# Kernel optimization log

Measured on AMD Instinct MI355X. Metric: run time of the kernel, lower is better.

The kernel has to match this reference:

```python
import jax, jax.numpy as jnp
import numpy as np

KCONV = 4
NSTATE = 64
NH_SPA = 4
NH_SPE = 8
NH_ATTN = 8
QLEN = 5


def _ln(x, w, b, eps=1e-5):
    mu = jnp.mean(x, -1, keepdims=True)
    var = jnp.var(x, -1, keepdims=True)
    return (x - mu) * jax.lax.rsqrt(var + eps) * w + b


def _sincos_2d(dim, H):
    # standard 2D sin-cos positional embedding, [H*H, dim]
    def e1(d, pos):
        omega = 1.0 / (10000.0 ** (np.arange(d // 2, dtype=np.float64) / (d / 2.0)))
        out = pos[:, None] * omega[None, :]
        return np.concatenate([np.sin(out), np.cos(out)], axis=-1)
    gh, gw = np.meshgrid(np.arange(H), np.arange(H), indexing='ij')
    emb = np.concatenate([e1(dim // 2, gh.reshape(-1)), e1(dim // 2, gw.reshape(-1))], axis=-1)
    return jnp.asarray(emb, jnp.float32)


def _ssd_scan(x, dt, A, Bm, Cm):
    # x:[b,l,h,p] dt:[b,l,h] A:[h] Bm,Cm:[b,l,n] (ngroups=1)
    b, l, h, p = x.shape
    dA = jnp.exp(dt * A)            # [b,l,h]
    dtx = dt[..., None] * x          # [b,l,h,p]

    def step(hs, inp):
        dA_t, dtx_t, B_t, C_t = inp
        hs = hs * dA_t[:, :, None, None] + dtx_t[..., None] * B_t[:, None, None, :]
        return hs, jnp.einsum('bhpn,bn->bhp', hs, C_t)

    h0 = jnp.zeros((b, h, p, Bm.shape[-1]), x.dtype)
    _, ys = jax.lax.scan(step, h0, (dA.transpose(1, 0, 2), dtx.transpose(1, 0, 2, 3),
                                    Bm.transpose(1, 0, 2), Cm.transpose(1, 0, 2)))
    return ys.transpose(1, 0, 2, 3)


def _mamba2(u, in_w, conv_w, conv_b, dt_bias, A_log, Dp, rms_w, out_w, nheads, n=NSTATE):
    # Mamba2 forward (d_state=64, d_conv=4, expand=2, rmsnorm gated, no biases on projections)
    b, l, _ = u.shape
    d_in_proj = in_w.shape[0]
    d_inner = (d_in_proj - 2 * n - nheads) // 2
    zxbcdt = u @ in_w.T
    z = zxbcdt[..., :d_inner]
    xBC = zxbcdt[..., d_inner:2 * d_inner + 2 * n]
    dt = jax.nn.softplus(zxbcdt[..., 2 * d_inner + 2 * n:] + dt_bias)  # [b,l,h]
    # causal depthwise conv1d, kernel 4
    xp = jnp.pad(xBC, ((0, 0), (KCONV - 1, 0), (0, 0)))
    xc = sum(xp[:, k:k + l, :] * conv_w[:, k] for k in range(KCONV)) + conv_b
    xBC = jax.nn.silu(xc)
    xh = xBC[..., :d_inner].reshape(b, l, nheads, -1)
    Bm = xBC[..., d_inner:d_inner + n]
    Cm = xBC[..., d_inner + n:]
    y = _ssd_scan(xh, dt, -jnp.exp(A_log), Bm, Cm)
    y = y + Dp[None, None, :, None] * xh
    y = y.reshape(b, l, -1) * jax.nn.silu(z)
    y = y * jax.lax.rsqrt(jnp.mean(y * y, -1, keepdims=True) + 1e-5) * rms_w
    return y @ out_w.T


def _forward(floats, sorted_index):
    (x, spa_ln_w, spa_ln_b, spa_in_w, spa_conv_w, spa_conv_b, spa_dt_bias, spa_A_log, spa_D,
     spa_rms_w, spa_out_w, spe_ln_w, spe_ln_b, spe_in_w, spe_conv_w, spe_conv_b, spe_dt_bias,
     spe_A_log, spe_D, spe_rms_w, spe_out_w, norm_w, norm_b, cprj_w, cprj_b,
     aq_w, aq_b, ak_w, ak_b, av_w, av_b, ao_w, ao_b,
     sq_w, sq_b, sk_w, sk_b, sv_w, sv_b, so_w, so_b,
     ds_conv_w, ds_ln_w, ds_ln_b) = floats
    b, c, H, W = x.shape
    # seq_generate: pos embed + reorder by (precomputed MST/BFS) sorted_index
    pe = _sincos_2d(c, H)                                  # [H*W, c]
    xs = x.transpose(0, 2, 3, 1).reshape(b, H * W, c) + pe[None]
    xs = jnp.take_along_axis(xs, sorted_index[..., None], axis=1)
    # SSD blocks
    for i in range(spa_ln_w.shape[0]):
        h1 = _mamba2(_ln(xs, spa_ln_w[i], spa_ln_b[i]), spa_in_w[i], spa_conv_w[i], spa_conv_b[i],
                     spa_dt_bias[i], spa_A_log[i], spa_D[i], spa_rms_w[i], spa_out_w[i], NH_SPA) + xs
        h2 = _mamba2(_ln(h1.transpose(0, 2, 1), spe_ln_w[i], spe_ln_b[i]), spe_in_w[i], spe_conv_w[i],
                     spe_conv_b[i], spe_dt_bias[i], spe_A_log[i], spe_D[i], spe_rms_w[i], spe_out_w[i], NH_SPE)
        xs = h2.transpose(0, 2, 1) + h1
    xs = _ln(xs, norm_w, norm_b)
    # center query: Conv1d(kernel=QLEN, pad=0) over the first QLEN tokens -> [b, c]
    center = jnp.einsum('blc,ocl->bo', xs[:, :QLEN, :], cprj_w) + cprj_b
    # Spa_Attention: center query attends over all tokens; per-token reweighting of V
    nh = NH_ATTN
    hd = c // nh
    q = (center @ aq_w.T + aq_b).reshape(b, nh, hd)
    k = (xs @ ak_w.T + ak_b).reshape(b, -1, nh, hd)
    v = (xs @ av_w.T + av_b).reshape(b, -1, nh, hd)
    attn = jax.nn.softmax(jnp.einsum('bhd,blhd->bhl', q, k) / float(np.sqrt(hd)), axis=-1)
    out = (v * attn.transpose(0, 2, 1)[..., None]).reshape(b, -1, c) @ ao_w.T + ao_b
    xs = xs + out
    # Spe_Attention: self-attention over channel tokens (dim = seq_len)
    xt = xs.transpose(0, 2, 1)                              # [b, c, L]
    q2 = xt @ sq_w.T + sq_b
    k2 = xt @ sk_w.T + sk_b
    v2 = xt @ sv_w.T + sv_b
    attn2 = jax.nn.softmax(jnp.einsum('bqd,bkd->bqk', q2, k2) / float(np.sqrt(xt.shape[-1])), axis=-1)
    xs = xs + ((attn2 @ v2) @ so_w.T + so_b).transpose(0, 2, 1)
    # Downsample: invert ordering, reshape to image, conv stride 2, LayerNorm
    inv = jnp.argsort(sorted_index, axis=1)
    xr = jnp.take_along_axis(xs, inv[..., None], axis=1).reshape(b, H, W, c)
    y = jax.lax.conv_general_dilated(xr, ds_conv_w, (2, 2), [(1, 1), (1, 1)],
                                     dimension_numbers=('NHWC', 'HWIO', 'NHWC'))
    return _ln(y, ds_ln_w, ds_ln_b)  # [b, H/2, W/2, c]


def setup_inputs() -> dict:
    key = jax.random.key(0)
    ks = iter(jax.random.split(key, 64))

    def rn(shape, s=0.02):
        return jax.random.normal(next(ks), shape, jnp.float32) * s

    d = {}
    d['x'] = jax.random.normal(next(ks), (16, 128, 16, 16), jnp.float32)
    d['sorted_index'] = jnp.argsort(jax.random.uniform(next(ks), (16, 256)), axis=1)
    d['spa_ln_w'] = jnp.ones((2, 128), jnp.float32)
    d['spa_ln_b'] = jnp.zeros((2, 128), jnp.float32)
    d['spa_in_w'] = rn((2, 644, 128))
    d['spa_conv_w'] = rn((2, 384, 4), 0.2)
    d['spa_conv_b'] = jnp.zeros((2, 384), jnp.float32)
    d['spa_dt_bias'] = rn((2, 4), 0.1) - 2.0
    d['spa_A_log'] = jnp.log(jax.random.uniform(next(ks), (2, 4), minval=1.0, maxval=8.0))
    d['spa_D'] = jnp.ones((2, 4), jnp.float32)
    d['spa_rms_w'] = jnp.ones((2, 256), jnp.float32)
    d['spa_out_w'] = rn((2, 128, 256))
    d['spe_ln_w'] = jnp.ones((2, 256), jnp.float32)
    d['spe_ln_b'] = jnp.zeros((2, 256), jnp.float32)
    d['spe_in_w'] = rn((2, 1160, 256))
    d['spe_conv_w'] = rn((2, 640, 4), 0.2)
    d['spe_conv_b'] = jnp.zeros((2, 640), jnp.float32)
    d['spe_dt_bias'] = rn((2, 8), 0.1) - 2.0
    d['spe_A_log'] = jnp.log(jax.random.uniform(next(ks), (2, 8), minval=1.0, maxval=8.0))
    d['spe_D'] = jnp.ones((2, 8), jnp.float32)
    d['spe_rms_w'] = jnp.ones((2, 512), jnp.float32)
    d['spe_out_w'] = rn((2, 256, 512))
    d['norm_w'] = jnp.ones((128,), jnp.float32)
    d['norm_b'] = jnp.zeros((128,), jnp.float32)
    d['cprj_w'] = rn((128, 128, 5), 0.05)
    d['cprj_b'] = jnp.zeros((128,), jnp.float32)
    for nm in ['aq', 'ak', 'av', 'ao']:
        d[nm + '_w'] = rn((128, 128), 0.05)
        d[nm + '_b'] = jnp.zeros((128,), jnp.float32)
    for nm in ['sq', 'sk', 'sv', 'so']:
        d[nm + '_w'] = rn((256, 256), 0.05)
        d[nm + '_b'] = jnp.zeros((256,), jnp.float32)
    d['ds_conv_w'] = rn((3, 3, 128, 128), 0.05)
    d['ds_ln_w'] = jnp.ones((128,), jnp.float32)
    d['ds_ln_b'] = jnp.zeros((128,), jnp.float32)
    return d


def reference(x, sorted_index, spa_ln_w, spa_ln_b, spa_in_w, spa_conv_w, spa_conv_b, spa_dt_bias,
              spa_A_log, spa_D, spa_rms_w, spa_out_w, spe_ln_w, spe_ln_b, spe_in_w, spe_conv_w,
              spe_conv_b, spe_dt_bias, spe_A_log, spe_D, spe_rms_w, spe_out_w, norm_w, norm_b,
              cprj_w, cprj_b, aq_w, aq_b, ak_w, ak_b, av_w, av_b, ao_w, ao_b,
              sq_w, sq_b, sk_w, sk_b, sv_w, sv_b, so_w, so_b, ds_conv_w, ds_ln_w, ds_ln_b):
    floats = (x, spa_ln_w, spa_ln_b, spa_in_w, spa_conv_w, spa_conv_b, spa_dt_bias, spa_A_log, spa_D,
              spa_rms_w, spa_out_w, spe_ln_w, spe_ln_b, spe_in_w, spe_conv_w, spe_conv_b, spe_dt_bias,
              spe_A_log, spe_D, spe_rms_w, spe_out_w, norm_w, norm_b, cprj_w, cprj_b,
              aq_w, aq_b, ak_w, ak_b, av_w, av_b, ao_w, ao_b,
              sq_w, sq_b, sk_w, sk_b, sv_w, sv_b, so_w, so_b, ds_conv_w, ds_ln_w, ds_ln_b)
    return _forward(floats, sorted_index)
```

## Files before the change

kernel.cpp:

```cpp
#include <hip/hip_runtime.h>
#include <math.h>

#define DEV __device__ __forceinline__

DEV float siluf(float x){ return x / (1.f + __expf(-x)); }
DEV float softplusf(float x){ return (x > 20.f) ? x : log1pf(__expf(x)); }

DEV void blk_sum2(float &a, float &b, float* sm){
    int lane = threadIdx.x & 63, wid = threadIdx.x >> 6, nw = blockDim.x >> 6;
    #pragma unroll
    for (int off = 32; off; off >>= 1){ a += __shfl_down(a, off); b += __shfl_down(b, off); }
    if (lane == 0){ sm[wid] = a; sm[8 + wid] = b; }
    __syncthreads();
    float ra = 0.f, rb = 0.f;
    for (int i = 0; i < nw; i++){ ra += sm[i]; rb += sm[8 + i]; }
    __syncthreads();
    a = ra; b = rb;
}
DEV float blk_sum1(float v, float* sm){
    int lane = threadIdx.x & 63, wid = threadIdx.x >> 6, nw = blockDim.x >> 6;
    #pragma unroll
    for (int off = 32; off; off >>= 1) v += __shfl_down(v, off);
    if (lane == 0) sm[wid] = v;
    __syncthreads();
    float r = 0.f;
    for (int i = 0; i < nw; i++) r += sm[i];
    __syncthreads();
    return r;
}
DEV float blk_max1(float v, float* sm){
    int lane = threadIdx.x & 63, wid = threadIdx.x >> 6, nw = blockDim.x >> 6;
    #pragma unroll
    for (int off = 32; off; off >>= 1) v = fmaxf(v, __shfl_down(v, off));
    if (lane == 0) sm[wid] = v;
    __syncthreads();
    float r = -3.4e38f;
    for (int i = 0; i < nw; i++) r = fmaxf(r, sm[i]);
    __syncthreads();
    return r;
}

DEV void tr_body(const float* __restrict__ ip, float* __restrict__ op,
                 int R, int C, int c0, int r0){
    __shared__ float tile[32][33];
    int tx = threadIdx.x & 31, ty = threadIdx.x >> 5;
    #pragma unroll
    for (int rr = ty; rr < 32; rr += 8)
        tile[rr][tx] = ip[(size_t)(r0 + rr) * C + c0 + tx];
    __syncthreads();
    #pragma unroll
    for (int rr = ty; rr < 32; rr += 8)
        op[(size_t)(c0 + rr) * R + r0 + tx] = tile[tx][rr];
}

__global__ __launch_bounds__(256) void k_tr(const float* __restrict__ in,
                                            float* __restrict__ out, int R, int C){
    tr_body(in + (size_t)blockIdx.z * R * C, out + (size_t)blockIdx.z * R * C,
            R, C, blockIdx.x * 32, blockIdx.y * 32);
}

__global__ __launch_bounds__(256) void k_tr_multi(const float* __restrict__ x,
        float* __restrict__ xT, const float* __restrict__ aow, float* __restrict__ owt,
        const float* __restrict__ sow, float* __restrict__ sowt){
    int idx = blockIdx.x;
    if (idx < 512){
        int bx = idx & 7, by = (idx >> 3) & 3, bz = idx >> 5;
        tr_body(x + (size_t)bz * 32768, xT + (size_t)bz * 32768, 128, 256, bx * 32, by * 32);
    } else if (idx < 528){
        int l = idx - 512;
        tr_body(aow, owt, 128, 128, (l & 3) * 32, (l >> 2) * 32);
    } else {
        int l = idx - 528;
        tr_body(sow, sowt, 256, 256, (l & 7) * 32, (l >> 3) * 32);
    }
}

__global__ void k_embed(const float* __restrict__ xT, const int* __restrict__ sidx,
                        float* __restrict__ xs){
    int bl = blockIdx.x; int b = bl >> 8; int c = threadIdx.x;
    int p = sidx[bl];
    int hh = p >> 4, ww = p & 15;
    int pos = (c < 64) ? hh : ww;
    int jm = c & 63;
    float om = __expf(-(float)(jm & 31) * 0.28782313662425574f);
    float ang = (float)pos * om;
    float pe = (jm < 32) ? sinf(ang) : cosf(ang);
    xs[(size_t)bl * 128 + c] = xT[((size_t)(b * 256 + p)) * 128 + c] + pe;
}

__global__ void k_ln(const float* __restrict__ in, const float* __restrict__ w,
                     const float* __restrict__ bb, float* __restrict__ out, int dim){
    __shared__ float sm[16];
    int row = blockIdx.x, t = threadIdx.x;
    float v = in[(size_t)row * dim + t];
    float a = v, q = v * v;
    blk_sum2(a, q, sm);
    float inv = 1.f / (float)dim;
    float mu = a * inv;
    float var = q * inv - mu * mu;
    float rs = rsqrtf(var + 1e-5f);
    out[(size_t)row * dim + t] = (v - mu) * rs * w[t] + bb[t];
}

__global__ __launch_bounds__(256) void k_gemm_ln(const float* __restrict__ A,
        const float* __restrict__ W, const float* __restrict__ lw,
        const float* __restrict__ lb, float* __restrict__ out, int N, int K){
    __shared__ float lds[2][32][68];
    int j0 = blockIdx.x * 64, r0 = blockIdx.y * 64;
    int tid = threadIdx.x;
    int cg = tid & 15, rg = tid >> 4;
    int row = tid >> 2, kg = tid & 3;
    int wrow = j0 + row; if (wrow > N - 1) wrow = N - 1;
    const float* Ar = A + (size_t)(r0 + row) * K;
    float s = 0.f, ss = 0.f;
    for (int k0 = 0; k0 < K; k0 += 32){
        float4 a0 = *(const float4*)(Ar + k0 + kg * 4);
        float4 a1 = *(const float4*)(Ar + k0 + 16 + kg * 4);
        s  += a0.x + a0.y + a0.z + a0.w + a1.x + a1.y + a1.z + a1.w;
        ss += a0.x*a0.x + a0.y*a0.y + a0.z*a0.z + a0.w*a0.w
            + a1.x*a1.x + a1.y*a1.y + a1.z*a1.z + a1.w*a1.w;
    }
    s  += __shfl_xor(s, 1);  ss += __shfl_xor(ss, 1);
    s  += __shfl_xor(s, 2);  ss += __shfl_xor(ss, 2);
    float inv = 1.f / (float)K;
    float mu = s * inv;
    float rs = rsqrtf(ss * inv - mu * mu + 1e-5f);
    float acc[4][4] = {};
    for (int k0 = 0; k0 < K; k0 += 32){
        float4 a0 = *(const float4*)(Ar + k0 + kg * 4);
        float4 a1 = *(const float4*)(Ar + k0 + 16 + kg * 4);
        float4 w0 = *(const float4*)(lw + k0 + kg * 4);
        float4 w1 = *(const float4*)(lw + k0 + 16 + kg * 4);
        float4 b0 = *(const float4*)(lb + k0 + kg * 4);
        float4 b1 = *(const float4*)(lb + k0 + 16 + kg * 4);
        const float* Wp = W + (size_t)wrow * K + k0 + kg * 4;
        float4 v0 = *(const float4*)(Wp);
        float4 v1 = *(const float4*)(Wp + 16);
        a0.x = (a0.x - mu) * rs * w0.x + b0.x; a0.y = (a0.y - mu) * rs * w0.y + b0.y;
        a0.z = (a0.z - mu) * rs * w0.z + b0.z; a0.w = (a0.w - mu) * rs * w0.w + b0.w;
        a1.x = (a1.x - mu) * rs * w1.x + b1.x; a1.y = (a1.y - mu) * rs * w1.y + b1.y;
        a1.z = (a1.z - mu) * rs * w1.z + b1.z; a1.w = (a1.w - mu) * rs * w1.w + b1.w;
        __syncthreads();
        lds[0][kg * 4 + 0][row] = a0.x; lds[0][kg * 4 + 1][row] = a0.y;
        lds[0][kg * 4 + 2][row] = a0.z; lds[0][kg * 4 + 3][row] = a0.w;
        lds[0][16 + kg * 4 + 0][row] = a1.x; lds[0][16 + kg * 4 + 1][row] = a1.y;
        lds[0][16 + kg * 4 + 2][row] = a1.z; lds[0][16 + kg * 4 + 3][row] = a1.w;
        lds[1][kg * 4 + 0][row] = v0.x; lds[1][kg * 4 + 1][row] = v0.y;
        lds[1][kg * 4 + 2][row] = v0.z; lds[1][kg * 4 + 3][row] = v0.w;
        lds[1][16 + kg * 4 + 0][row] = v1.x; lds[1][16 + kg * 4 + 1][row] = v1.y;
        lds[1][16 + kg * 4 + 2][row] = v1.z; lds[1][16 + kg * 4 + 3][row] = v1.w;
        __syncthreads();
        #pragma unroll
        for (int kk = 0; kk < 32; kk++){
            float4 a4 = *(const float4*)(&lds[0][kk][rg << 2]);
            float4 w4 = *(const float4*)(&lds[1][kk][cg << 2]);
            float av_[4] = {a4.x, a4.y, a4.z, a4.w};
            float wv_[4] = {w4.x, w4.y, w4.z, w4.w};
            #pragma unroll
            for (int ri = 0; ri < 4; ri++)
                #pragma unroll
                for (int ci = 0; ci < 4; ci++)
                    acc[ri][ci] = fmaf(av_[ri], wv_[ci], acc[ri][ci]);
        }
    }
    #pragma unroll
    for (int ri = 0; ri < 4; ri++){
        int r = r0 + (rg << 2) + ri;
        int j = j0 + (cg << 2);
        if (j < N){
            float4 v = make_float4(acc[ri][0], acc[ri][1], acc[ri][2], acc[ri][3]);
            *(float4*)(&out[(size_t)r * N + j]) = v;
        }
    }
}

__global__ __launch_bounds__(256) void k_gemm_gate(const float* __restrict__ Y,
        const float* __restrict__ Z, const float* __restrict__ rw,
        const float* __restrict__ W, const float* __restrict__ res,
        float* __restrict__ out, int N, int K, int zs, int mode){
    __shared__ float lds[2][32][68];
    __shared__ float sscale[64];
    int j0 = blockIdx.x * 64, r0 = blockIdx.y * 64;
    int tid = threadIdx.x;
    int cg = tid & 15, rg = tid >> 4;
    int row = tid >> 2, kg = tid & 3;
    const float* Yr = Y + (size_t)(r0 + row) * K;
    const float* Zr = Z + (size_t)(r0 + row) * zs;
    float ssq = 0.f;
    float acc[4][4] = {};
    for (int k0 = 0; k0 < K; k0 += 32){
        float4 y0 = *(const float4*)(Yr + k0 + kg * 4);
        float4 y1 = *(const float4*)(Yr + k0 + 16 + kg * 4);
        float4 z0 = *(const float4*)(Zr + k0 + kg * 4);
        float4 z1 = *(const float4*)(Zr + k0 + 16 + kg * 4);
        float4 g0 = *(const float4*)(rw + k0 + kg * 4);
        float4 g1 = *(const float4*)(rw + k0 + 16 + kg * 4);
        const float* Wp = W + (size_t)(j0 + row) * K + k0 + kg * 4;
        float4 v0 = *(const float4*)(Wp);
        float4 v1 = *(const float4*)(Wp + 16);
        y0.x *= siluf(z0.x); y0.y *= siluf(z0.y); y0.z *= siluf(z0.z); y0.w *= siluf(z0.w);
        y1.x *= siluf(z1.x); y1.y *= siluf(z1.y); y1.z *= siluf(z1.z); y1.w *= siluf(z1.w);
        ssq += y0.x*y0.x + y0.y*y0.y + y0.z*y0.z + y0.w*y0.w
             + y1.x*y1.x + y1.y*y1.y + y1.z*y1.z + y1.w*y1.w;
        y0.x *= g0.x; y0.y *= g0.y; y0.z *= g0.z; y0.w *= g0.w;
        y1.x *= g1.x; y1.y *= g1.y; y1.z *= g1.z; y1.w *= g1.w;
        __syncthreads();
        lds[0][kg * 4 + 0][row] = y0.x; lds[0][kg * 4 + 1][row] = y0.y;
        lds[0][kg * 4 + 2][row] = y0.z; lds[0][kg * 4 + 3][row] = y0.w;
        lds[0][16 + kg * 4 + 0][row] = y1.x; lds[0][16 + kg * 4 + 1][row] = y1.y;
        lds[0][16 + kg * 4 + 2][row] = y1.z; lds[0][16 + kg * 4 + 3][row] = y1.w;
        lds[1][kg * 4 + 0][row] = v0.x; lds[1][kg * 4 + 1][row] = v0.y;
        lds[1][kg * 4 + 2][row] = v0.z; lds[1][kg * 4 + 3][row] = v0.w;
        lds[1][16 + kg * 4 + 0][row] = v1.x; lds[1][16 + kg * 4 + 1][row] = v1.y;
        lds[1][16 + kg * 4 + 2][row] = v1.z; lds[1][16 + kg * 4 + 3][row] = v1.w;
        __syncthreads();
        #pragma unroll
        for (int kk = 0; kk < 32; kk++){
            float4 a4 = *(const float4*)(&lds[0][kk][rg << 2]);
            float4 w4 = *(const float4*)(&lds[1][kk][cg << 2]);
            float av_[4] = {a4.x, a4.y, a4.z, a4.w};
            float wv_[4] = {w4.x, w4.y, w4.z, w4.w};
            #pragma unroll
            for (int ri = 0; ri < 4; ri++)
                #pragma unroll
                for (int ci = 0; ci < 4; ci++)
                    acc[ri][ci] = fmaf(av_[ri], wv_[ci], acc[ri][ci]);
        }
    }
    ssq += __shfl_xor(ssq, 1);
    ssq += __shfl_xor(ssq, 2);
    if ((tid & 3) == 0) sscale[row] = rsqrtf(ssq / (float)K + 1e-5f);
    __syncthreads();
    if (mode == 2){
        float (*T)[68] = (float (*)[68])lds;
        #pragma unroll
        for (int ri = 0; ri < 4; ri++){
            float sc = sscale[(rg << 2) + ri];
            #pragma unroll
            for (int ci = 0; ci < 4; ci++)
                T[(cg << 2) + ci][(rg << 2) + ri] = acc[ri][ci] * sc;
        }
        __syncthreads();
        int b2 = r0 >> 7, ii0 = r0 & 127;
        int jj = tid >> 2, seg = tid & 3;
        size_t base = ((size_t)(b2 * 256 + j0 + jj)) * 128 + ii0 + seg * 16;
        float* op = out + base;
        const float* rp = res + base;
        #pragma unroll
        for (int c = 0; c < 4; c++){
            float4 v = *(const float4*)(&T[jj][seg * 16 + c * 4]);
            float4 rv = *(const float4*)(rp + c * 4);
            v.x += rv.x; v.y += rv.y; v.z += rv.z; v.w += rv.w;
            *(float4*)(op + c * 4) = v;
        }
    } else {
        #pragma unroll
        for (int ri = 0; ri < 4; ri++){
            int r = r0 + (rg << 2) + ri;
            int j = j0 + (cg << 2);
            float sc = sscale[(rg << 2) + ri];
            float4 v = make_float4(acc[ri][0] * sc, acc[ri][1] * sc,
                                   acc[ri][2] * sc, acc[ri][3] * sc);
            float4 rv = *(const float4*)(&res[(size_t)r * N + j]);
            v.x += rv.x; v.y += rv.y; v.z += rv.z; v.w += rv.w;
            *(float4*)(&out[(size_t)r * N + j]) = v;
        }
    }
}

DEV void gemm_core(const float* __restrict__ A, const float* __restrict__ W,
                   const float* __restrict__ bias, float* __restrict__ out,
                   int N, int K, int mode, int j0, int r0){
    __shared__ float lds[2][32][68];
    int tid = threadIdx.x;
    int cg = tid & 15, rg = tid >> 4;
    int row = tid >> 2, kg = tid & 3;
    int wrow = j0 + row; if (wrow > N - 1) wrow = N - 1;
    float acc[4][4] = {};
    for (int k0 = 0; k0 < K; k0 += 32){
        const float* Ap = A + (size_t)(r0 + row) * K + k0 + kg * 4;
        float4 a0 = *(const float4*)(Ap);
        float4 a1 = *(const float4*)(Ap + 16);
        const float* Wp = W + (size_t)wrow * K + k0 + kg * 4;
        float4 w0 = *(const float4*)(Wp);
        float4 w1 = *(const float4*)(Wp + 16);
        __syncthreads();
        lds[0][kg * 4 + 0][row] = a0.x; lds[0][kg * 4 + 1][row] = a0.y;
        lds[0][kg * 4 + 2][row] = a0.z; lds[0][kg * 4 + 3][row] = a0.w;
        lds[0][16 + kg * 4 + 0][row] = a1.x; lds[0][16 + kg * 4 + 1][row] = a1.y;
        lds[0][16 + kg * 4 + 2][row] = a1.z; lds[0][16 + kg * 4 + 3][row] = a1.w;
        lds[1][kg * 4 + 0][row] = w0.x; lds[1][kg * 4 + 1][row] = w0.y;
        lds[1][kg * 4 + 2][row] = w0.z; lds[1][kg * 4 + 3][row] = w0.w;
        lds[1][16 + kg * 4 + 0][row] = w1.x; lds[1][16 + kg * 4 + 1][row] = w1.y;
        lds[1][16 + kg * 4 + 2][row] = w1.z; lds[1][16 + kg * 4 + 3][row] = w1.w;
        __syncthreads();
        #pragma unroll
        for (int kk = 0; kk < 32; kk++){
            float4 a4 = *(const float4*)(&lds[0][kk][rg << 2]);
            float4 w4 = *(const float4*)(&lds[1][kk][cg << 2]);
            float av_[4] = {a4.x, a4.y, a4.z, a4.w};
            float wv_[4] = {w4.x, w4.y, w4.z, w4.w};
            #pragma unroll
            for (int ri = 0; ri < 4; ri++)
                #pragma unroll
                for (int ci = 0; ci < 4; ci++)
                    acc[ri][ci] = fmaf(av_[ri], wv_[ci], acc[ri][ci]);
        }
    }
    if (mode == 3){
        float (*T)[68] = (float (*)[68])lds;
        __syncthreads();
        #pragma unroll
        for (int ri = 0; ri < 4; ri++)
            #pragma unroll
            for (int ci = 0; ci < 4; ci++)
                T[(cg << 2) + ci][(rg << 2) + ri] = acc[ri][ci];
        __syncthreads();
        int b2 = r0 >> 7, ii0 = r0 & 127;
        int jj = tid >> 2, seg = tid & 3;
        size_t base = ((size_t)(b2 * 256 + j0 + jj)) * 128 + ii0 + seg * 16;
        float* op = out + base;
        float bj = bias[j0 + jj];
        #pragma unroll
        for (int c = 0; c < 4; c++){
            float4 v = *(const float4*)(&T[jj][seg * 16 + c * 4]);
            v.x += bj; v.y += bj; v.z += bj; v.w += bj;
            *(float4*)(op + c * 4) = v;
        }
    } else {
        #pragma unroll
        for (int ri = 0; ri < 4; ri++){
            int r = r0 + (rg << 2) + ri;
            int j = j0 + (cg << 2);
            float4 v = make_float4(acc[ri][0], acc[ri][1], acc[ri][2], acc[ri][3]);
            v.x += bias[j]; v.y += bias[j + 1]; v.z += bias[j + 2]; v.w += bias[j + 3];
            *(float4*)(&out[(size_t)r * N + j]) = v;
        }
    }
}

struct GJob { const float* W; const float* bias; float* out; int mode; };

__global__ __launch_bounds__(256) void k_gemm3(const float* __restrict__ A,
                                               GJob ja, GJob jb, GJob jc,
                                               int N, int K){
    GJob j = (blockIdx.z == 0) ? ja : ((blockIdx.z == 1) ? jb : jc);
    gemm_core(A, j.W, j.bias, j.out, N, K, j.mode, blockIdx.x * 64, blockIdx.y * 64);
}

__global__ void k_conv(const float* __restrict__ zx, const float* __restrict__ cw,
                       const float* __restrict__ cb, float* __restrict__ xc,
                       const float* __restrict__ dtbias, const float* __restrict__ Al,
                       float* __restrict__ dt, float* __restrict__ dlA,
                       int L, int D, int stride, int off, int nh, int dtoff){
    int bl = blockIdx.x;
    int l = bl & (L - 1);
    const float* base = zx + (size_t)bl * stride + off;
    for (int d = threadIdx.x; d < D; d += blockDim.x){
        float acc = cb[d];
        #pragma unroll
        for (int k = 0; k < 4; k++){
            int dl = l + k - 3;
            if (dl >= 0) acc += base[(ptrdiff_t)(k - 3) * stride + d] * cw[d * 4 + k];
        }
        xc[(size_t)bl * D + d] = siluf(acc);
    }
    int t = threadIdx.x;
    if (t < nh){
        float xv = zx[(size_t)bl * stride + dtoff + t] + dtbias[t];
        float d = softplusf(xv);
        dt[(size_t)bl * nh + t] = d;
        dlA[(size_t)bl * nh + t] = -d * __expf(Al[t]);
    }
}

__global__ __launch_bounds__(256) void k_ssd_chunk(
        const float* __restrict__ xc, const float* __restrict__ dt,
        const float* __restrict__ dlA, float* __restrict__ y,
        float* __restrict__ S, float* __restrict__ clb,
        int L, int nh, int nc, int xcs, int bo, int co, int ys){
    __shared__ float sX[64][68];
    __shared__ float sB[64][68];
    __shared__ float sC[64][68];
    __shared__ float cl[64], sdt[64], sw[64];
    int blk = blockIdx.x;
    int c = blk % nc; int bh = blk / nc; int h = bh % nh; int b = bh / nh;
    int l0 = c * 64;
    int tid = threadIdx.x;
    const float* base = xc + ((size_t)(b * L + l0)) * xcs;
    for (int idx = tid; idx < 4096; idx += 256){
        int s = idx >> 6, n = idx & 63;
        const float* row = base + (size_t)s * xcs;
        sX[s][n] = row[h * 64 + n];
        sB[s][n] = row[bo + n];
        sC[s][n] = row[co + n];
    }
    if (tid < 64){
        size_t di = (size_t)(b * L + l0 + tid) * nh + h;
        float dlv = dlA[di];
        sdt[tid] = dt[di];
// ... 260 lines not shown
        for (int ii = 0; ii < 8; ii++)
            sa[ii][t] = (lgp[0][ii][t] + lgp[1][ii][t]) * (1.f / 16.f);
    }
    __syncthreads();
    if (t < 8){
        float mx = -3.4e38f;
        for (int j = 0; j < 128; j++) mx = fmaxf(mx, sa[t][j]);
        float sm = 0.f;
        for (int j = 0; j < 128; j++) sm += __expf(sa[t][j] - mx);
        mxs[t] = mx; sms[t] = 1.f / sm;
    }
    __syncthreads();
    if (t < 128){
        #pragma unroll
        for (int ii = 0; ii < 8; ii++)
            sa[ii][t] = __expf(sa[ii][t] - mxs[ii]) * sms[ii];
    }
    __syncthreads();
    {
        float acc[8] = {};
        const float* vb = v2 + (size_t)b * 32768 + t;
        for (int j = 0; j < 128; j++){
            float vv = vb[(size_t)j * 256];
            #pragma unroll
            for (int ii = 0; ii < 8; ii++) acc[ii] = fmaf(sa[ii][j], vv, acc[ii]);
        }
        #pragma unroll
        for (int ii = 0; ii < 8; ii++) av[ii][t] = acc[ii];
    }
    __syncthreads();
    float acc[8] = {};
    for (int d = 0; d < 256; d++){
        float wv = sowt[d * 256 + t];
        #pragma unroll
        for (int ii = 0; ii < 8; ii++) acc[ii] = fmaf(av[ii][d], wv, acc[ii]);
    }
    float bias = sob[t];
    int p = sidx[b * 256 + t];
    const float* xin = xs + ((size_t)(b * 256 + t)) * 128 + i0;
    float* xout = xr + ((size_t)(b * 256 + p)) * 128 + i0;
    #pragma unroll
    for (int ii = 0; ii < 8; ii++) xout[ii] = xin[ii] + acc[ii] + bias;
}

__global__ __launch_bounds__(256) void k_conv_gemm(const float* __restrict__ xr,
                                                   const float* __restrict__ W2,
                                                   float* __restrict__ part){
    __shared__ float As[16][68];
    __shared__ float Ws[16][64];
    int j0 = blockIdx.x * 64, r0 = blockIdx.y * 64, s = blockIdx.z;
    int tid = threadIdx.x;
    int cg = tid & 15, rg = tid >> 4;
    int arow = tid >> 2, akg = tid & 3;
    int r = r0 + arow; int b = r >> 6, oh = (r >> 3) & 7, ow = r & 7;
    float acc[4][4] = {};
    int kbeg = s * 288, kend = kbeg + 288;
    for (int k0 = kbeg; k0 < kend; k0 += 16){
        {
            int k = k0 + akg * 4;
            int khw = k >> 7, c = k & 127;
            int kh = khw / 3, kw = khw - kh * 3;
            int ih = oh * 2 - 1 + kh, iw = ow * 2 - 1 + kw;
            float4 a4 = make_float4(0.f, 0.f, 0.f, 0.f);
            if (ih >= 0 && ih < 16 && iw >= 0 && iw < 16)
                a4 = *(const float4*)(xr + ((size_t)((b << 8) + (ih << 4) + iw)) * 128 + c);
            As[akg * 4 + 0][arow] = a4.x; As[akg * 4 + 1][arow] = a4.y;
            As[akg * 4 + 2][arow] = a4.z; As[akg * 4 + 3][arow] = a4.w;
        }
        #pragma unroll
        for (int it = 0; it < 4; it++){
            int idx = tid + it * 256;
            int jj = idx & 63, kk = idx >> 6;
            Ws[kk][jj] = W2[(size_t)(k0 + kk) * 128 + j0 + jj];
        }
        __syncthreads();
        #pragma unroll
        for (int kk = 0; kk < 16; kk++){
            float4 a4 = *(const float4*)(&As[kk][rg << 2]);
            float4 w4 = *(const float4*)(&Ws[kk][cg << 2]);
            float av_[4] = {a4.x, a4.y, a4.z, a4.w};
            float wv_[4] = {w4.x, w4.y, w4.z, w4.w};
            #pragma unroll
            for (int ri = 0; ri < 4; ri++)
                #pragma unroll
                for (int ci = 0; ci < 4; ci++)
                    acc[ri][ci] = fmaf(av_[ri], wv_[ci], acc[ri][ci]);
        }
        __syncthreads();
    }
    float* pp = part + (size_t)s * 1024 * 128;
    #pragma unroll
    for (int ri = 0; ri < 4; ri++){
        int rr = r0 + (rg << 2) + ri;
        #pragma unroll
        for (int ci = 0; ci < 4; ci++){
            int j = j0 + (cg << 2) + ci;
            pp[(size_t)rr * 128 + j] = acc[ri][ci];
        }
    }
}

__global__ void k_part_ln(const float* __restrict__ part, const float* __restrict__ lnw,
                          const float* __restrict__ lnb, float* __restrict__ out){
    __shared__ float sm[16];
    int r = blockIdx.x, t = threadIdx.x;
    float v = part[(size_t)r * 128 + t]
            + part[(size_t)(1024 + r) * 128 + t]
            + part[(size_t)(2048 + r) * 128 + t]
            + part[(size_t)(3072 + r) * 128 + t];
    float a = v, q = v * v;
    blk_sum2(a, q, sm);
    float mu = a * (1.f / 128.f);
    float var = q * (1.f / 128.f) - mu * mu;
    float rs = rsqrtf(var + 1e-5f);
    out[(size_t)r * 128 + t] = (v - mu) * rs * lnw[t] + lnb[t];
}

extern "C" void kernel_launch(void* const* d_in, const int* in_sizes, int n_in,
                              void* d_out, int out_size, void* d_ws, size_t ws_size,
                              hipStream_t stream) {
    const float* x          = (const float*)d_in[0];
    const int*   sidx       = (const int*)  d_in[1];
    const float* spa_ln_w   = (const float*)d_in[2];
    const float* spa_ln_b   = (const float*)d_in[3];
    const float* spa_in_w   = (const float*)d_in[4];
    const float* spa_conv_w = (const float*)d_in[5];
    const float* spa_conv_b = (const float*)d_in[6];
    const float* spa_dt_bias= (const float*)d_in[7];
    const float* spa_A_log  = (const float*)d_in[8];
    const float* spa_D      = (const float*)d_in[9];
    const float* spa_rms_w  = (const float*)d_in[10];
    const float* spa_out_w  = (const float*)d_in[11];
    const float* spe_ln_w   = (const float*)d_in[12];
    const float* spe_ln_b   = (const float*)d_in[13];
    const float* spe_in_w   = (const float*)d_in[14];
    const float* spe_conv_w = (const float*)d_in[15];
    const float* spe_conv_b = (const float*)d_in[16];
    const float* spe_dt_bias= (const float*)d_in[17];
    const float* spe_A_log  = (const float*)d_in[18];
    const float* spe_D      = (const float*)d_in[19];
    const float* spe_rms_w  = (const float*)d_in[20];
// ... 106 lines not shown
```

Baseline: 639.4 us.

## Use bf16 MFMA in projection GEMMs and prefetch conv GEMM tiles

Replaces the FP32 scalar-FMA inner loops of the LN-fused GEMM, the gated RMSNorm GEMM and the three-way QKV GEMM with bf16 MFMA 16x16x32 matrix instructions. Operands are converted to bf16 in shared memory, the K step is widened to 64, and the epilogues are remapped to the MFMA accumulator layout. Separately, the downsample conv GEMM now uses register prefetch of the next A/W tile and float4 weight loads. The bf16 conversion lowers GEMM input precision and may loosen numerical accuracy against the FP32 reference.

After: 549.0 us. -14.1%, faster.

```diff
diff --git a/kernel.cpp b/kernel.cpp
--- a/kernel.cpp
+++ b/kernel.cpp
@@ -3,8 +3,21 @@
 
 #define DEV __device__ __forceinline__
 
+typedef __attribute__((ext_vector_type(8))) short short8;
+typedef __attribute__((ext_vector_type(4))) float f32x4;
+typedef unsigned short ushort_t;
+typedef unsigned int uint_t;
+
 DEV float siluf(float x){ return x / (1.f + __expf(-x)); }
 DEV float softplusf(float x){ return (x > 20.f) ? x : log1pf(__expf(x)); }
+
+DEV ushort_t bf16r(float f){
+    uint_t u = __float_as_uint(f);
+    return (ushort_t)((u + 0x7fffu + ((u >> 16) & 1u)) >> 16);
+}
+DEV uint_t pack2(float a, float b){
+    return (uint_t)bf16r(a) | ((uint_t)bf16r(b) << 16);
+}
 
 DEV void blk_sum2(float &a, float &b, float* sm){
     int lane = threadIdx.x & 63, wid = threadIdx.x >> 6, nw = blockDim.x >> 6;
@@ -102,16 +115,19 @@
     out[(size_t)row * dim + t] = (v - mu) * rs * w[t] + bb[t];
 }
 
+
 __global__ __launch_bounds__(256) void k_gemm_ln(const float* __restrict__ A,
         const float* __restrict__ W, const float* __restrict__ lw,
         const float* __restrict__ lb, float* __restrict__ out, int N, int K){
-    __shared__ float lds[2][32][68];
+    __shared__ __align__(16) ushort_t smem[2 * 64 * 72];
+    ushort_t (*Abf)[72] = (ushort_t (*)[72])smem;
+    ushort_t (*Wbf)[72] = (ushort_t (*)[72])(smem + 64 * 72);
     int j0 = blockIdx.x * 64, r0 = blockIdx.y * 64;
     int tid = threadIdx.x;
-    int cg = tid & 15, rg = tid >> 4;
     int row = tid >> 2, kg = tid & 3;
     int wrow = j0 + row; if (wrow > N - 1) wrow = N - 1;
     const float* Ar = A + (size_t)(r0 + row) * K;
+    const float* Wr = W + (size_t)wrow * K;
     float s = 0.f, ss = 0.f;
     for (int k0 = 0; k0 < K; k0 += 32){
         float4 a0 = *(const float4*)(Ar + k0 + kg * 4);
@@ -125,51 +141,61 @@
     float inv = 1.f / (float)K;
     float mu = s * inv;
     float rs = rsqrtf(ss * inv - mu * mu + 1e-5f);
-    float acc[4][4] = {};
-    for (int k0 = 0; k0 < K; k0 += 32){
-        float4 a0 = *(const float4*)(Ar + k0 + kg * 4);
-        float4 a1 = *(const float4*)(Ar + k0 + 16 + kg * 4);
-        float4 w0 = *(const float4*)(lw + k0 + kg * 4);
-        float4 w1 = *(const float4*)(lw + k0 + 16 + kg * 4);
-        float4 b0 = *(const float4*)(lb + k0 + kg * 4);
-        float4 b1 = *(const float4*)(lb + k0 + 16 + kg * 4);
-        const float* Wp = W + (size_t)wrow * K + k0 + kg * 4;
-        float4 v0 = *(const float4*)(Wp);
-        float4 v1 = *(const float4*)(Wp + 16);
-        a0.x = (a0.x - mu) * rs * w0.x + b0.x; a0.y = (a0.y - mu) * rs * w0.y + b0.y;
-        a0.z = (a0.z - mu) * rs * w0.z + b0.z; a0.w = (a0.w - mu) * rs * w0.w + b0.w;
-        a1.x = (a1.x - mu) * rs * w1.x + b1.x; a1.y = (a1.y - mu) * rs * w1.y + b1.y;
-        a1.z = (a1.z - mu) * rs * w1.z + b1.z; a1.w = (a1.w - mu) * rs * w1.w + b1.w;
-        __syncthreads();
-        lds[0][kg * 4 + 0][row] = a0.x; lds[0][kg * 4 + 1][row] = a0.y;
-        lds[0][kg * 4 + 2][row] = a0.z; lds[0][kg * 4 + 3][row] = a0.w;
-        lds[0][16 + kg * 4 + 0][row] = a1.x; lds[0][16 + kg * 4 + 1][row] = a1.y;
-        lds[0][16 + kg * 4 + 2][row] = a1.z; lds[0][16 + kg * 4 + 3][row] = a1.w;
-        lds[1][kg * 4 + 0][row] = v0.x; lds[1][kg * 4 + 1][row] = v0.y;
-        lds[1][kg * 4 + 2][row] = v0.z; lds[1][kg * 4 + 3][row] = v0.w;
-        lds[1][16 + kg * 4 + 0][row] = v1.x; lds[1][16 + kg * 4 + 1][row] = v1.y;
-        lds[1][16 + kg * 4 + 2][row] = v1.z; lds[1][16 + kg * 4 + 3][row] = v1.w;
-        __syncthreads();
-        #pragma unroll
-        for (int kk = 0; kk < 32; kk++){
-            float4 a4 = *(const float4*)(&lds[0][kk][rg << 2]);
-            float4 w4 = *(const float4*)(&lds[1][kk][cg << 2]);
-            float av_[4] = {a4.x, a4.y, a4.z, a4.w};
-            float wv_[4] = {w4.x, w4.y, w4.z, w4.w};
-            #pragma unroll
-            for (int ri = 0; ri < 4; ri++)
-                #pragma unroll
-                for (int ci = 0; ci < 4; ci++)
-                    acc[ri][ci] = fmaf(av_[ri], wv_[ci], acc[ri][ci]);
-        }
-    }
-    #pragma unroll
-    for (int ri = 0; ri < 4; ri++){
-        int r = r0 + (rg << 2) + ri;
-        int j = j0 + (cg << 2);
+    int wv = tid >> 6, lane = tid & 63, lm = lane & 15, quad = lane >> 4;
+    f32x4 zero4 = {0.f, 0.f, 0.f, 0.f};
+    f32x4 acc[4] = {zero4, zero4, zero4, zero4};
+    for (int kc0 = 0; kc0 < K; kc0 += 64){
+        int kb = kc0 + kg * 16;
+        float4 q[4], g[4], b[4], p[4];
+        #pragma unroll
+        for (int i = 0; i < 4; i++){
+            q[i] = *(const float4*)(Ar + kb + i * 4);
+            g[i] = *(const float4*)(lw + kb + i * 4);
+            b[i] = *(const float4*)(lb + kb + i * 4);
+            p[i] = *(const float4*)(Wr + kb + i * 4);
+        }
+        #pragma unroll
+        for (int i = 0; i < 4; i++){
+            q[i].x = (q[i].x - mu) * rs * g[i].x + b[i].x;
+            q[i].y = (q[i].y - mu) * rs * g[i].y + b[i].y;
+            q[i].z = (q[i].z - mu) * rs * g[i].z + b[i].z;
+            q[i].w = (q[i].w - mu) * rs * g[i].w + b[i].w;
+        }
+        __syncthreads();
+        {
+            uint4 u0, u1;
+            u0.x = pack2(q[0].x, q[0].y); u0.y = pack2(q[0].z, q[0].w);
+            u0.z = pack2(q[1].x, q[1].y); u0.w = pack2(q[1].z, q[1].w);
+            u1.x = pack2(q[2].x, q[2].y); u1.y = pack2(q[2].z, q[2].w);
+            u1.z = pack2(q[3].x, q[3].y); u1.w = pack2(q[3].z, q[3].w);
+            *(uint4*)&Abf[row][kg * 16] = u0;
+            *(uint4*)&Abf[row][kg * 16 + 8] = u1;
+            u0.x = pack2(p[0].x, p[0].y); u0.y = pack2(p[0].z, p[0].w);
+            u0.z = pack2(p[1].x, p[1].y); u0.w = pack2(p[1].z, p[1].w);
+            u1.x = pack2(p[2].x, p[2].y); u1.y = pack2(p[2].z, p[2].w);
+            u1.z = pack2(p[3].x, p[3].y); u1.w = pack2(p[3].z, p[3].w);
+            *(uint4*)&Wbf[row][kg * 16] = u0;
+            *(uint4*)&Wbf[row][kg * 16 + 8] = u1;
+        }
+        __syncthreads();
+        #pragma unroll
+        for (int kk = 0; kk < 64; kk += 32){
+            short8 af = *(const short8*)&Abf[wv * 16 + lm][kk + quad * 8];
+            #pragma unroll
+            for (int c = 0; c < 4; c++){
+                short8 bfv = *(const short8*)&Wbf[c * 16 + lm][kk + quad * 8];
+                acc[c] = __builtin_amdgcn_mfma_f32_16x16x32_bf16(af, bfv, acc[c], 0, 0, 0);
+            }
+        }
+    }
+    int rbase = r0 + wv * 16 + quad * 4;
+    #pragma unroll
+    for (int c = 0; c < 4; c++){
+        int j = j0 + c * 16 + lm;
         if (j < N){
-            float4 v = make_float4(acc[ri][0], acc[ri][1], acc[ri][2], acc[ri][3]);
-            *(float4*)(&out[(size_t)r * N + j]) = v;
+            #pragma unroll
+            for (int reg = 0; reg < 4; reg++)
+                out[(size_t)(rbase + reg) * N + j] = acc[c][reg];
         }
     }
 }
@@ -178,68 +204,79 @@
         const float* __restrict__ Z, const float* __restrict__ rw,
         const float* __restrict__ W, const float* __restrict__ res,
         float* __restrict__ out, int N, int K, int zs, int mode){
-    __shared__ float lds[2][32][68];
+    __shared__ __align__(16) ushort_t smem[2 * 64 * 72];
+    ushort_t (*Abf)[72] = (ushort_t (*)[72])smem;
+    ushort_t (*Wbf)[72] = (ushort_t (*)[72])(smem + 64 * 72);
     __shared__ float sscale[64];
     int j0 = blockIdx.x * 64, r0 = blockIdx.y * 64;
     int tid = threadIdx.x;
-    int cg = tid & 15, rg = tid >> 4;
     int row = tid >> 2, kg = tid & 3;
     const float* Yr = Y + (size_t)(r0 + row) * K;
     const float* Zr = Z + (size_t)(r0 + row) * zs;
+    const float* Wr = W + (size_t)(j0 + row) * K;
+    int wv = tid >> 6, lane = tid & 63, lm = lane & 15, quad = lane >> 4;
     float ssq = 0.f;
-    float acc[4][4] = {};
-    for (int k0 = 0; k0 < K; k0 += 32){
-        float4 y0 = *(const float4*)(Yr + k0 + kg * 4);
-        float4 y1 = *(const float4*)(Yr + k0 + 16 + kg * 4);
-        float4 z0 = *(const float4*)(Zr + k0 + kg * 4);
-        float4 z1 = *(const float4*)(Zr + k0 + 16 + kg * 4);
-        float4 g0 = *(const float4*)(rw + k0 + kg * 4);
-        float4 g1 = *(const float4*)(rw + k0 + 16 + kg * 4);
-        const float* Wp = W + (size_t)(j0 + row) * K + k0 + kg * 4;
-        float4 v0 = *(const float4*)(Wp);
-        float4 v1 = *(const float4*)(Wp + 16);
-        y0.x *= siluf(z0.x); y0.y *= siluf(z0.y); y0.z *= siluf(z0.z); y0.w *= siluf(z0.w);
-        y1.x *= siluf(z1.x); y1.y *= siluf(z1.y); y1.z *= siluf(z1.z); y1.w *= siluf(z1.w);
-        ssq += y0.x*y0.x + y0.y*y0.y + y0.z*y0.z + y0.w*y0.w
-             + y1.x*y1.x + y1.y*y1.y + y1.z*y1.z + y1.w*y1.w;
-        y0.x *= g0.x; y0.y *= g0.y; y0.z *= g0.z; y0.w *= g0.w;
-        y1.x *= g1.x; y1.y *= g1.y; y1.z *= g1.z; y1.w *= g1.w;
-        __syncthreads();
-        lds[0][kg * 4 + 0][row] = y0.x; lds[0][kg * 4 + 1][row] = y0.y;
-        lds[0][kg * 4 + 2][row] = y0.z; lds[0][kg * 4 + 3][row] = y0.w;
-        lds[0][16 + kg * 4 + 0][row] = y1.x; lds[0][16 + kg * 4 + 1][row] = y1.y;
-        lds[0][16 + kg * 4 + 2][row] = y1.z; lds[0][16 + kg * 4 + 3][row] = y1.w;
-        lds[1][kg * 4 + 0][row] = v0.x; lds[1][kg * 4 + 1][row] = v0.y;
-        lds[1][kg * 4 + 2][row] = v0.z; lds[1][kg * 4 + 3][row] = v0.w;
-        lds[1][16 + kg * 4 + 0][row] = v1.x; lds[1][16 + kg * 4 + 1][row] = v1.y;
-        lds[1][16 + kg * 4 + 2][row] = v1.z; lds[1][16 + kg * 4 + 3][row] = v1.w;
-        __syncthreads();
-        #pragma unroll
-        for (int kk = 0; kk < 32; kk++){
-            float4 a4 = *(const float4*)(&lds[0][kk][rg << 2]);
-            float4 w4 = *(const float4*)(&lds[1][kk][cg << 2]);
-            float av_[4] = {a4.x, a4.y, a4.z, a4.w};
-            float wv_[4] = {w4.x, w4.y, w4.z, w4.w};
-            #pragma unroll
-            for (int ri = 0; ri < 4; ri++)
-                #pragma unroll
-                for (int ci = 0; ci < 4; ci++)
-                    acc[ri][ci] = fmaf(av_[ri], wv_[ci], acc[ri][ci]);
+    f32x4 zero4 = {0.f, 0.f, 0.f, 0.f};
+    f32x4 acc[4] = {zero4, zero4, zero4, zero4};
+    for (int kc0 = 0; kc0 < K; kc0 += 64){
+        int kb = kc0 + kg * 16;
+        float4 y[4], z[4], g[4], p[4];
+        #pragma unroll
+        for (int i = 0; i < 4; i++){
+            y[i] = *(const float4*)(Yr + kb + i * 4);
+            z[i] = *(const float4*)(Zr + kb + i * 4);
+            g[i] = *(const float4*)(rw + kb + i * 4);
+            p[i] = *(const float4*)(Wr + kb + i * 4);
+        }
+        #pragma unroll
+        for (int i = 0; i < 4; i++){
+            y[i].x *= siluf(z[i].x); y[i].y *= siluf(z[i].y);
+            y[i].z *= siluf(z[i].z); y[i].w *= siluf(z[i].w);
+            ssq += y[i].x*y[i].x + y[i].y*y[i].y + y[i].z*y[i].z + y[i].w*y[i].w;
+            y[i].x *= g[i].x; y[i].y *= g[i].y; y[i].z *= g[i].z; y[i].w *= g[i].w;
+        }
+        __syncthreads();
+        {
+            uint4 u0, u1;
+            u0.x = pack2(y[0].x, y[0].y); u0.y = pack2(y[0].z, y[0].w);
+            u0.z = pack2(y[1].x, y[1].y); u0.w = pack2(y[1].z, y[1].w);
+            u1.x = pack2(y[2].x, y[2].y); u1.y = pack2(y[2].z, y[2].w);
+            u1.z = pack2(y[3].x, y[3].y); u1.w = pack2(y[3].z, y[3].w);
+            *(uint4*)&Abf[row][kg * 16] = u0;
+            *(uint4*)&Abf[row][kg * 16 + 8] = u1;
+            u0.x = pack2(p[0].x, p[0].y); u0.y = pack2(p[0].z, p[0].w);
+            u0.z = pack2(p[1].x, p[1].y); u0.w = pack2(p[1].z, p[1].w);
+            u1.x = pack2(p[2].x, p[2].y); u1.y = pack2(p[2].z, p[2].w);
+            u1.z = pack2(p[3].x, p[3].y); u1.w = pack2(p[3].z, p[3].w);
+            *(uint4*)&Wbf[row][kg * 16] = u0;
+            *(uint4*)&Wbf[row][kg * 16 + 8] = u1;
+        }
+        __syncthreads();
+        #pragma unroll
+        for (int kk = 0; kk < 64; kk += 32){
+            short8 af = *(const short8*)&Abf[wv * 16 + lm][kk + quad * 8];
+            #pragma unroll
+            for (int c = 0; c < 4; c++){
+                short8 bfv = *(const short8*)&Wbf[c * 16 + lm][kk + quad * 8];
+                acc[c] = __builtin_amdgcn_mfma_f32_16x16x32_bf16(af, bfv, acc[c], 0, 0, 0);
+            }
         }
     }
     ssq += __shfl_xor(ssq, 1);
     ssq += __shfl_xor(ssq, 2);
-    if ((tid & 3) == 0) sscale[row] = rsqrtf(ssq / (float)K + 1e-5f);
-    __syncthreads();
+    if (kg == 0) sscale[row] = rsqrtf(ssq / (float)K + 1e-5f);
+    __syncthreads();
+    int lr0 = wv * 16 + quad * 4;
+    float scr[4];
+    #pragma unroll
+    for (int reg = 0; reg < 4; reg++) scr[reg] = sscale[lr0 + reg];
     if (mode == 2){
-        float (*T)[68] = (float (*)[68])lds;
-        #pragma unroll
-        for (int ri = 0; ri < 4; ri++){
-            float sc = sscale[(rg << 2) + ri];
-            #pragma unroll
-            for (int ci = 0; ci < 4; ci++)
-                T[(cg << 2) + ci][(rg << 2) + ri] = acc[ri][ci] * sc;
-        }
+        float (*T)[68] = (float (*)[68])smem;
+        #pragma unroll
+        for (int c = 0; c < 4; c++)
+            #pragma unroll
+            for (int reg = 0; reg < 4; reg++)
+                T[c * 16 + lm][lr0 + reg] = acc[c][reg] * scr[reg];
         __syncthreads();
         int b2 = r0 >> 7, ii0 = r0 & 127;
         int jj = tid >> 2, seg = tid & 3;
@@ -254,67 +291,84 @@
             *(float4*)(op + c * 4) = v;
         }
     } else {
-        #pragma unroll
-        for (int ri = 0; ri < 4; ri++){
-            int r = r0 + (rg << 2) + ri;
-            int j = j0 + (cg << 2);
-            float sc = sscale[(rg << 2) + ri];
-            float4 v = make_float4(acc[ri][0] * sc, acc[ri][1] * sc,
-                                   acc[ri][2] * sc, acc[ri][3] * sc);
-            float4 rv = *(const float4*)(&res[(size_t)r * N + j]);
-            v.x += rv.x; v.y += rv.y; v.z += rv.z; v.w += rv.w;
-            *(float4*)(&out[(size_t)r * N + j]) = v;
-        }
-    }
-}
-
-DEV void gemm_core(const float* __restrict__ A, const float* __restrict__ W,
-                   const float* __restrict__ bias, float* __restrict__ out,
-                   int N, int K, int mode, int j0, int r0){
-    __shared__ float lds[2][32][68];
+        int rbase = r0 + lr0;
+        #pragma unroll
+        for (int c = 0; c < 4; c++){
+            int j = j0 + c * 16 + lm;
+            #pragma unroll
+            for (int reg = 0; reg < 4; reg++){
+                size_t oi = (size_t)(rbase + reg) * N + j;
+                out[oi] = acc[c][reg] * scr[reg] + res[oi];
+            }
+        }
+    }
+}
+
+struct GJob { const float* W; const float* bias; float* out; int mode; };
+
+__global__ __launch_bounds__(256) void k_gemm3(const float* __restrict__ A,
+                                               GJob ja, GJob jb, GJob jc,
+                                               int N, int K){
+    GJob job = (blockIdx.z == 0) ? ja : ((blockIdx.z == 1) ? jb : jc);
+    const float* W = job.W;
+    const float* bias = job.bias;
+    float* out = job.out;
+    int mode = job.mode;
+    __shared__ __align__(16) ushort_t smem[2 * 64 * 72];
+    ushort_t (*Abf)[72] = (ushort_t (*)[72])smem;
+    ushort_t (*Wbf)[72] = (ushort_t (*)[72])(smem + 64 * 72);
+    int j0 = blockIdx.x * 64, r0 = blockIdx.y * 64;
     int tid = threadIdx.x;
-    int cg = tid & 15, rg = tid >> 4;
     int row = tid >> 2, kg = tid & 3;
-    int wrow = j0 + row; if (wrow > N - 1) wrow = N - 1;
-    float acc[4][4] = {};
-    for (int k0 = 0; k0 < K; k0 += 32){
-        const float* Ap = A + (size_t)(r0 + row) * K + k0 + kg * 4;
-        float4 a0 = *(const float4*)(Ap);
-        float4 a1 = *(const float4*)(Ap + 16);
-        const float* Wp = W + (size_t)wrow * K + k0 + kg * 4;
-        float4 w0 = *(const float4*)(Wp);
-        float4 w1 = *(const float4*)(Wp + 16);
-        __syncthreads();
-        lds[0][kg * 4 + 0][row] = a0.x; lds[0][kg * 4 + 1][row] = a0.y;
-        lds[0][kg * 4 + 2][row] = a0.z; lds[0][kg * 4 + 3][row] = a0.w;
-        lds[0][16 + kg * 4 + 0][row] = a1.x; lds[0][16 + kg * 4 + 1][row] = a1.y;
-        lds[0][16 + kg * 4 + 2][row] = a1.z; lds[0][16 + kg * 4 + 3][row] = a1.w;
-        lds[1][kg * 4 + 0][row] = w0.x; lds[1][kg * 4 + 1][row] = w0.y;
-        lds[1][kg * 4 + 2][row] = w0.z; lds[1][kg * 4 + 3][row] = w0.w;
-        lds[1][16 + kg * 4 + 0][row] = w1.x; lds[1][16 + kg * 4 + 1][row] = w1.y;
-        lds[1][16 + kg * 4 + 2][row] = w1.z; lds[1][16 + kg * 4 + 3][row] = w1.w;
-        __syncthreads();
-        #pragma unroll
-        for (int kk = 0; kk < 32; kk++){
-            float4 a4 = *(const float4*)(&lds[0][kk][rg << 2]);
-            float4 w4 = *(const float4*)(&lds[1][kk][cg << 2]);
-            float av_[4] = {a4.x, a4.y, a4.z, a4.w};
-            float wv_[4] = {w4.x, w4.y, w4.z, w4.w};
-            #pragma unroll
-            for (int ri = 0; ri < 4; ri++)
-                #pragma unroll
-                for (int ci = 0; ci < 4; ci++)
-                    acc[ri][ci] = fmaf(av_[ri], wv_[ci], acc[ri][ci]);
-        }
-    }
+    const float* Ar = A + (size_t)(r0 + row) * K;
+    const float* Wr = W + (size_t)(j0 + row) * K;
+    int wv = tid >> 6, lane = tid & 63, lm = lane & 15, quad = lane >> 4;
+    f32x4 zero4 = {0.f, 0.f, 0.f, 0.f};
+    f32x4 acc[4] = {zero4, zero4, zero4, zero4};
+    for (int kc0 = 0; kc0 < K; kc0 += 64){
+        int kb = kc0 + kg * 16;
+        float4 q[4], p[4];
+        #pragma unroll
+        for (int i = 0; i < 4; i++){
+            q[i] = *(const float4*)(Ar + kb + i * 4);
+            p[i] = *(const float4*)(Wr + kb + i * 4);
+        }
+        __syncthreads();
+        {
+            uint4 u0, u1;
+            u0.x = pack2(q[0].x, q[0].y); u0.y = pack2(q[0].z, q[0].w);
+            u0.z = pack2(q[1].x, q[1].y); u0.w = pack2(q[1].z, q[1].w);
+            u1.x = pack2(q[2].x, q[2].y); u1.y = pack2(q[2].z, q[2].w);
+            u1.z = pack2(q[3].x, q[3].y); u1.w = pack2(q[3].z, q[3].w);
+            *(uint4*)&Abf[row][kg * 16] = u0;
+            *(uint4*)&Abf[row][kg * 16 + 8] = u1;
+            u0.x = pack2(p[0].x, p[0].y); u0.y = pack2(p[0].z, p[0].w);
+            u0.z = pack2(p[1].x, p[1].y); u0.w = pack2(p[1].z, p[1].w);
+            u1.x = pack2(p[2].x, p[2].y); u1.y = pack2(p[2].z, p[2].w);
+            u1.z = pack2(p[3].x, p[3].y); u1.w = pack2(p[3].z, p[3].w);
+            *(uint4*)&Wbf[row][kg * 16] = u0;
+            *(uint4*)&Wbf[row][kg * 16 + 8] = u1;
+        }
+        __syncthreads();
+        #pragma unroll
+        for (int kk = 0; kk < 64; kk += 32){
+            short8 af = *(const short8*)&Abf[wv * 16 + lm][kk + quad * 8];
+            #pragma unroll
+            for (int c = 0; c < 4; c++){
+                short8 bfv = *(const short8*)&Wbf[c * 16 + lm][kk + quad * 8];
+                acc[c] = __builtin_amdgcn_mfma_f32_16x16x32_bf16(af, bfv, acc[c], 0, 0, 0);
+            }
+        }
+    }
+    int lr0 = wv * 16 + quad * 4;
     if (mode == 3){
-        float (*T)[68] = (float (*)[68])lds;
-        __syncthreads();
-        #pragma unroll
-        for (int ri = 0; ri < 4; ri++)
-            #pragma unroll
-            for (int ci = 0; ci < 4; ci++)
-                T[(cg << 2) + ci][(rg << 2) + ri] = acc[ri][ci];
+        __syncthreads();
+        float (*T)[68] = (float (*)[68])smem;
+        #pragma unroll
+        for (int c = 0; c < 4; c++)
+            #pragma unroll
+            for (int reg = 0; reg < 4; reg++)
+                T[c * 16 + lm][lr0 + reg] = acc[c][reg];
         __syncthreads();
         int b2 = r0 >> 7, ii0 = r0 & 127;
         int jj = tid >> 2, seg = tid & 3;
@@ -328,24 +382,16 @@
             *(float4*)(op + c * 4) = v;
         }
     } else {
-        #pragma unroll
-        for (int ri = 0; ri < 4; ri++){
-            int r = r0 + (rg << 2) + ri;
-            int j = j0 + (cg << 2);
-            float4 v = make_float4(acc[ri][0], acc[ri][1], acc[ri][2], acc[ri][3]);
-            v.x += bias[j]; v.y += bias[j + 1]; v.z += bias[j + 2]; v.w += bias[j + 3];
-            *(float4*)(&out[(size_t)r * N + j]) = v;
-        }
-    }
-}
-
-struct GJob { const float* W; const float* bias; float* out; int mode; };
-
-__global__ __launch_bounds__(256) void k_gemm3(const float* __restrict__ A,
-                                               GJob ja, GJob jb, GJob jc,
-                                               int N, int K){
-    GJob j = (blockIdx.z == 0) ? ja : ((blockIdx.z == 1) ? jb : jc);
-    gemm_core(A, j.W, j.bias, j.out, N, K, j.mode, blockIdx.x * 64, blockIdx.y * 64);
+        int rbase = r0 + lr0;
+        #pragma unroll
+        for (int c = 0; c < 4; c++){
+            int j = j0 + c * 16 + lm;
+            float bj = bias[j];
+            #pragma unroll
+            for (int reg = 0; reg < 4; reg++)
+                out[(size_t)(rbase + reg) * N + j] = acc[c][reg] + bj;
+        }
+    }
 }
 
 __global__ void k_conv(const float* __restrict__ zx, const float* __restrict__ cw,
@@ -712,41 +758,53 @@
     int tid = threadIdx.x;
     int cg = tid & 15, rg = tid >> 4;
     int arow = tid >> 2, akg = tid & 3;
+    int wkk = tid >> 4, wseg = tid & 15;
     int r = r0 + arow; int b = r >> 6, oh = (r >> 3) & 7, ow = r & 7;
     float acc[4][4] = {};
     int kbeg = s * 288, kend = kbeg + 288;
+    float4 a4, w4;
+    {
+        int k = kbeg + akg * 4;
+        int khw = k >> 7, c = k & 127;
+        int kh = khw / 3, kw = khw - kh * 3;
+        int ih = oh * 2 - 1 + kh, iw = ow * 2 - 1 + kw;
+        a4 = make_float4(0.f, 0.f, 0.f, 0.f);
+        if (ih >= 0 && ih < 16 && iw >= 0 && iw < 16)
+            a4 = *(const float4*)(xr + ((size_t)((b << 8) + (ih << 4) + iw)) * 128 + c);
+        w4 = *(const float4*)(W2 + (size_t)(kbeg + wkk) * 128 + j0 + wseg * 4);
+    }
     for (int k0 = kbeg; k0 < kend; k0 += 16){
-        {
-            int k = k0 + akg * 4;
+        __syncthreads();
+        As[akg * 4 + 0][arow] = a4.x; As[akg * 4 + 1][arow] = a4.y;
+        As[akg * 4 + 2][arow] = a4.z; As[akg * 4 + 3][arow] = a4.w;
+        Ws[wkk][wseg * 4 + 0] = w4.x; Ws[wkk][wseg * 4 + 1] = w4.y;
+        Ws[wkk][wseg * 4 + 2] = w4.z; Ws[wkk][wseg * 4 + 3] = w4.w;
+        __syncthreads();
+        bool more = (k0 + 16 < kend);
+        float4 na4, nw4;
+        if (more){
+            int k = k0 + 16 + akg * 4;
             int khw = k >> 7, c = k & 127;
             int kh = khw / 3, kw = khw - kh * 3;
             int ih = oh * 2 - 1 + kh, iw = ow * 2 - 1 + kw;
-            float4 a4 = make_float4(0.f, 0.f, 0.f, 0.f);
+            na4 = make_float4(0.f, 0.f, 0.f, 0.f);
             if (ih >= 0 && ih < 16 && iw >= 0 && iw < 16)
-                a4 = *(const float4*)(xr + ((size_t)((b << 8) + (ih << 4) + iw)) * 128 + c);
-            As[akg * 4 + 0][arow] = a4.x; As[akg * 4 + 1][arow] = a4.y;
-            As[akg * 4 + 2][arow] = a4.z; As[akg * 4 + 3][arow] = a4.w;
-        }
-        #pragma unroll
-        for (int it = 0; it < 4; it++){
-            int idx = tid + it * 256;
-            int jj = idx & 63, kk = idx >> 6;
-            Ws[kk][jj] = W2[(size_t)(k0 + kk) * 128 + j0 + jj];
-        }
-        __syncthreads();
+                na4 = *(const float4*)(xr + ((size_t)((b << 8) + (ih << 4) + iw)) * 128 + c);
+            nw4 = *(const float4*)(W2 + (size_t)(k0 + 16 + wkk) * 128 + j0 + wseg * 4);
+        }
         #pragma unroll
         for (int kk = 0; kk < 16; kk++){
-            float4 a4 = *(const float4*)(&As[kk][rg << 2]);
-            float4 w4 = *(const float4*)(&Ws[kk][cg << 2]);
-            float av_[4] = {a4.x, a4.y, a4.z, a4.w};
-            float wv_[4] = {w4.x, w4.y, w4.z, w4.w};
+            float4 av4 = *(const float4*)(&As[kk][rg << 2]);
+            float4 wv4 = *(const float4*)(&Ws[kk][cg << 2]);
+            float av_[4] = {av4.x, av4.y, av4.z, av4.w};
+            float wv_[4] = {wv4.x, wv4.y, wv4.z, wv4.w};
             #pragma unroll
             for (int ri = 0; ri < 4; ri++)
                 #pragma unroll
                 for (int ci = 0; ci < 4; ci++)
                     acc[ri][ci] = fmaf(av_[ri], wv_[ci], acc[ri][ci]);
         }
-        __syncthreads();
+        if (more){ a4 = na4; w4 = nw4; }
     }
     float* pp = part + (size_t)s * 1024 * 128;
     #pragma unroll
```
